# Performance work log

Hardware: AMD Instinct MI355X
Metric: run time of the kernel (lower is better)

## Reference

```python
import jax, jax.numpy as jnp
import numpy as np

B, T, E, D, OUT = 128, 64, 256, 256, 1  # batch, timesteps, encoder_hidden, decoder_hidden, out_feats


def setup_inputs() -> dict:
    key = jax.random.key(0)
    ks = jax.random.split(key, 14)
    s = 0.05
    return {
        "input_encoded": jax.random.normal(ks[0], (B, T, E), jnp.float32),
        "y_history": jax.random.normal(ks[1], (B, T - 1, OUT), jnp.float32),
        # attn_layer: Linear(2D+E -> E), Tanh, Linear(E -> 1)
        "W_a1": jax.random.normal(ks[2], (E, 2 * D + E), jnp.float32) * s,
        "b_a1": jax.random.normal(ks[3], (E,), jnp.float32) * s,
        "W_a2": jax.random.normal(ks[4], (1, E), jnp.float32) * s,
        "b_a2": jax.random.normal(ks[5], (1,), jnp.float32) * s,
        # fc: Linear(E + out_feats -> out_feats)
        "W_fc": jax.random.normal(ks[6], (OUT, E + OUT), jnp.float32) * s,
        "b_fc": jax.random.normal(ks[7], (OUT,), jnp.float32) * s,
        # LSTM(input_size=out_feats, hidden_size=D), gate order i,f,g,o
        "W_ih": jax.random.normal(ks[8], (4 * D, OUT), jnp.float32) * s,
        "W_hh": jax.random.normal(ks[9], (4 * D, D), jnp.float32) * s,
        "b_ih": jax.random.normal(ks[10], (4 * D,), jnp.float32) * s,
        "b_hh": jax.random.normal(ks[11], (4 * D,), jnp.float32) * s,
        # fc_final: Linear(D + E -> 2) (probabilistic=True)
        "W_ff": jax.random.normal(ks[12], (2, D + E), jnp.float32) * s,
        "b_ff": jax.random.normal(ks[13], (2,), jnp.float32) * s,
    }


def reference(input_encoded, y_history, W_a1, b_a1, W_a2, b_a2, W_fc, b_fc,
              W_ih, W_hh, b_ih, b_hh, W_ff, b_ff):
    Bn, Tn, En = input_encoded.shape
    Dn = W_hh.shape[1]

    def step(carry, y_t):
        h, c, _ = carry  # h, c: [B, D]
        # concat(hidden, cell, enc) broadcast over the T encoder positions -> [B, T, 2D+E]
        feats = jnp.concatenate([
            jnp.broadcast_to(h[:, None, :], (Bn, Tn, Dn)),
            jnp.broadcast_to(c[:, None, :], (Bn, Tn, Dn)),
            input_encoded,
        ], axis=2)
        scores = jnp.tanh(feats @ W_a1.T + b_a1) @ W_a2.T + b_a2  # [B, T, 1]
        attn = jax.nn.softmax(scores[..., 0], axis=1)              # [B, T]
        context = jnp.einsum('bt,bte->be', attn, input_encoded)   # [B, E]
        y_tilde = jnp.concatenate([context, y_t], axis=1) @ W_fc.T + b_fc  # [B, 1]
        # single LSTM step, PyTorch gate order (i, f, g, o)
        gates = y_tilde @ W_ih.T + b_ih + h @ W_hh.T + b_hh       # [B, 4D]
        i, f, g, o = jnp.split(gates, 4, axis=1)
        c_new = jax.nn.sigmoid(f) * c + jax.nn.sigmoid(i) * jnp.tanh(g)
        h_new = jax.nn.sigmoid(o) * jnp.tanh(c_new)
        return (h_new, c_new, context), None

    h0 = jnp.zeros((Bn, Dn), input_encoded.dtype)
    c0 = jnp.zeros((Bn, Dn), input_encoded.dtype)
    ctx0 = jnp.zeros((Bn, En), input_encoded.dtype)
    # data_integration=True: loop runs T-1 steps over y_history
    (h, c, context), _ = jax.lax.scan(step, (h0, c0, ctx0), jnp.swapaxes(y_history, 0, 1))
    return jnp.concatenate([h, context], axis=1) @ W_ff.T + b_ff  # [B, 2]
```

## Files before the change

### kernel.cpp

```cpp
#include <hip/hip_runtime.h>
#include <math.h>

#define BATCH 128
#define TENC  64
#define NSTEP 63

#define OFF_WA1ET  0
#define OFF_EPT    65536
#define OFF_PKH    2162688
#define OFF_SX     2359296
#define OFF_HX     2375680
#define OFF_FLAGS  2408448

#define SF 0
#define AF 1
#define CF 2
#define GF 3

typedef __attribute__((ext_vector_type(8))) _Float16 h8_t;
typedef __attribute__((ext_vector_type(2))) _Float16 h2_t;

#if defined(__has_builtin)
#if __has_builtin(__builtin_amdgcn_fdot2)
#define FDOT2(a, b, c) __builtin_amdgcn_fdot2((a), (b), (c), false)
#endif
#endif
#ifndef FDOT2
#define FDOT2(a, b, c) ((c) + (float)(a)[0] * (float)(b)[0] + (float)(a)[1] * (float)(b)[1])
#endif

__device__ __forceinline__ h2_t h2of(h8_t v, int i) {
    h2_t r = {v[2 * i], v[2 * i + 1]};
    return r;
}
__device__ __forceinline__ float ftanh(float x) {
    x = fminf(15.f, fmaxf(-15.f, x));
    float e = __expf(2.f * x);
    return (e - 1.f) * __builtin_amdgcn_rcpf(e + 1.f);
}
__device__ __forceinline__ float fsig(float x) {
    return __builtin_amdgcn_rcpf(1.f + __expf(-x));
}
__device__ __forceinline__ unsigned pack_hc(float h, float c) {
    unsigned short hu = __builtin_bit_cast(unsigned short, (_Float16)h);
    unsigned short cu = __builtin_bit_cast(unsigned short, (_Float16)c);
    return (unsigned)hu | ((unsigned)cu << 16);
}
#define FENCE() asm volatile("" ::: "memory")
#define LGKM0() asm volatile("s_waitcnt lgkmcnt(0)" ::: "memory")

__global__ void pack_weights(const float* __restrict__ Wa1,
                             const float* __restrict__ Whh,
                             float* __restrict__ ws) {
    int idx = blockIdx.x * blockDim.x + threadIdx.x;
    _Float16* PKH = (_Float16*)(ws + OFF_PKH);
    if (idx < 131072) {
        int m = idx & 7, j7 = (idx >> 3) & 127, it = (idx >> 10) & 7;
        int seg = (idx >> 13) & 1, kc = (idx >> 14) & 3, hp = (idx >> 16) & 1;
        int owner = seg ? (1 - hp) : hp;
        int idx256 = kc * 64 + it * 8 + m;
        int k = (idx256 < 128) ? owner * 128 + idx256
                               : 256 + owner * 128 + (idx256 - 128);
        int j = hp * 128 + j7;
        PKH[idx] = (_Float16)Wa1[j * 768 + k];
    } else if (idx < 393216) {
        int n = idx - 131072;
        int m = n & 7, qp = (n >> 3) & 511, kh = (n >> 12) & 1, kk = (n >> 13) & 15, h1 = n >> 17;
        int q = ((qp >> 7) << 8) + h1 * 128 + (qp & 127);
        int k = kh * 128 + kk * 8 + m;
        PKH[131072 + n] = (_Float16)Whh[q * 256 + k];
    } else if (idx < 458752) {
        int n = idx - 393216;
        int k = n >> 8, j = n & 255;
        ws[OFF_WA1ET + n] = Wa1[j * 768 + 512 + k];
    }
}

__global__ void zero_flags(float* __restrict__ ws) {
    unsigned* f = (unsigned*)(ws + OFF_FLAGS);
    f[threadIdx.x] = 0u;
}

__global__ void enc_proj_kernel(const float* __restrict__ enc,
                                const float* __restrict__ ba1,
                                float* __restrict__ ws) {
    __shared__ float smem[8448];
    const int b  = blockIdx.x >> 1;
    const int th = blockIdx.x & 1;
    const int t0 = th * 32;
    const int tid = threadIdx.x;

    const float* encb = enc + (b * TENC + t0) * 256;
    for (int c = 0; c < 32; ++c) smem[c * 256 + tid] = encb[c * 256 + tid];
    __syncthreads();

    const int w = tid >> 6, l = tid & 63;
    float acc[8][4];
    #pragma unroll
    for (int a = 0; a < 8; ++a)
        #pragma unroll
        for (int c = 0; c < 4; ++c) acc[a][c] = 0.f;

    const float4* WT = (const float4*)(ws + OFF_WA1ET);
    for (int k = 0; k < 256; ++k) {
        float4 wv = WT[k * 64 + l];
        #pragma unroll
        for (int tt = 0; tt < 8; ++tt) {
            float e = smem[(w * 8 + tt) * 256 + k];
            acc[tt][0] += e * wv.x; acc[tt][1] += e * wv.y;
            acc[tt][2] += e * wv.z; acc[tt][3] += e * wv.w;
        }
    }
    float4 bb = ((const float4*)ba1)[l];
    __syncthreads();
    #pragma unroll
    for (int tt = 0; tt < 8; ++tt) {
        smem[(4 * l + 0) * 33 + w * 8 + tt] = acc[tt][0] + bb.x;
        smem[(4 * l + 1) * 33 + w * 8 + tt] = acc[tt][1] + bb.y;
        smem[(4 * l + 2) * 33 + w * 8 + tt] = acc[tt][2] + bb.z;
        smem[(4 * l + 3) * 33 + w * 8 + tt] = acc[tt][3] + bb.w;
    }
    __syncthreads();
    float* EPT = ws + OFF_EPT + b * 16384;
    for (int c = 0; c < 32; ++c) {
        int i = c * 256 + tid;
        int j = i >> 5, t5 = i & 31;
        EPT[j * 64 + t0 + t5] = smem[j * 33 + t5];
    }
}

__global__ __launch_bounds__(1024, 4) void decoder_main(
    const float* __restrict__ enc, const float* __restrict__ yhist,
    const float* __restrict__ Wa2,
    const float* __restrict__ Wfc, const float* __restrict__ bfc,
    const float* __restrict__ wih, const float* __restrict__ bih,
    const float* __restrict__ bhh,
    const float* __restrict__ Wff, const float* __restrict__ bff,
    float* __restrict__ ws, float* __restrict__ out) {

    __shared__ float hc[512];
    __shared__ _Float16 hcf16[512] __attribute__((aligned(16)));
    __shared__ float red1[512];
    __shared__ float red2[512];
    __shared__ float g2[512];
    __shared__ float attnw[64];
    __shared__ float encw[64];
    __shared__ float wa2s[128];
    __shared__ float ys[64];
    __shared__ unsigned fl[4];
    __shared__ h8_t  wc[7168] __attribute__((aligned(16)));
    __shared__ float epl[8192];

    const int bid  = blockIdx.x;
    const int b    = bid & 127;
    const int h1   = bid >> 7;
    const int tid  = threadIdx.x;

    const _Float16* PKH = (const _Float16*)(ws + OFF_PKH);
    const float* EPTb = ws + OFF_EPT + b * 16384 + h1 * 8192;
    const float* encb = enc + b * 16384;

    if (tid < 512) { hc[tid] = 0.f; hcf16[tid] = (_Float16)0.f; }
    if (tid < 128) wa2s[tid] = Wa2[h1 * 128 + tid];
    if (tid < NSTEP) ys[tid] = yhist[b * NSTEP + tid];
    if (tid < 4) fl[tid] = 0u;
    {
        float* scr = (float*)wc;
        const int t = tid >> 4, cch = tid & 15;
        float p = 0.f;
        #pragma unroll
        for (int i = 0; i < 16; ++i)
            p += encb[t * 256 + cch * 16 + i] * Wfc[cch * 16 + i];
        scr[t * 16 + cch] = p;
    }
    __syncthreads();
    if (tid < 64) {
        float s = 0.f;
        #pragma unroll
        for (int c = 0; c < 16; ++c) s += ((float*)wc)[tid * 16 + c];
        encw[tid] = s;
    }
    __syncthreads();
    #pragma unroll
    for (int i = 0; i < 8; ++i) epl[i * 1024 + tid] = EPTb[i * 1024 + tid];
    const h8_t* PKGown = (const h8_t*)(PKH + 131072) + h1 * 16384;
    #pragma unroll
    for (int kk = 0; kk < 7; ++kk) wc[kk * 1024 + tid] = PKGown[kk * 1024 + tid];
    const float bfc0  = bfc[0];
    const float wfc_y = Wfc[256];
    float wii = 0.f, wif = 0.f, wig = 0.f, wio = 0.f;
    float bsi = 0.f, bsf = 0.f, bsg = 0.f, bso = 0.f;
    if (tid < 128) {
        const int q0 = h1 * 128 + tid;
        wii = wih[q0];       bsi = bih[q0]       + bhh[q0];
        wif = wih[256 + q0]; bsf = bih[256 + q0] + bhh[256 + q0];
        wig = wih[512 + q0]; bsg = bih[512 + q0] + bhh[512 + q0];
        wio = wih[768 + q0]; bso = bih[768 + q0] + bhh[768 + q0];
    }
    __syncthreads();

    const int j7 = tid & 127, kc = (tid >> 7) & 3;
    const h8_t* W1a = (const h8_t*)PKH + ((h1 * 4 + kc) * 2 + 0) * 1024 + j7;
    const h8_t* W1b = W1a + 1024;
    const _Float16* hb_own  = hcf16 + ((kc < 2) ? h1 * 128 + kc * 64
                                                : 256 + h1 * 128 + (kc - 2) * 64);
    const _Float16* hb_peer = hcf16 + ((kc < 2) ? (1 - h1) * 128 + kc * 64
                                                : 256 + (1 - h1) * 128 + (kc - 2) * 64);
    const h8_t* W4 = PKGown + (tid - 512);

    float*    SXown  = ws + OFF_SX + (b * 2 + h1) * 64;
    float*    SXpeer = ws + OFF_SX + (b * 2 + (1 - h1)) * 64;
    unsigned* HXown  = (unsigned*)(ws + OFF_HX) + (b * 2 + h1) * 128;
    unsigned* HXpeer = (unsigned*)(ws + OFF_HX) + (b * 2 + (1 - h1)) * 128;
    unsigned* FLGown  = (unsigned*)(ws + OFF_FLAGS) + (b * 2 + h1) * 2;
    unsigned* FLGpeer = (unsigned*)(ws + OFF_FLAGS) + (b * 2 + (1 - h1)) * 2;

    for (int step = 0; step < NSTEP; ++step) {
        const unsigned tgt = (unsigned)(step + 1);
        if (tid < 512) {
            float a0 = 0.f, a1 = 0.f;
            #pragma unroll 4
            for (int it = 0; it < 8; ++it) {
                h8_t w  = W1a[it * 128];
                h8_t hv = *(const h8_t*)(hb_own + it * 8);
                a0 = FDOT2(h2of(w, 0), h2of(hv, 0), a0);
                a1 = FDOT2(h2of(w, 1), h2of(hv, 1), a1);
                a0 = FDOT2(h2of(w, 2), h2of(hv, 2), a0);
                a1 = FDOT2(h2of(w, 3), h2of(hv, 3), a1);
            }
            if (step) {
                while (atomicAdd(&fl[SF], 0u) < 2u * (unsigned)step)
                    __builtin_amdgcn_s_sleep(1);
                FENCE();
            }
            #pragma unroll 4
            for (int it = 0; it < 8; ++it) {
                h8_t w  = W1b[it * 128];
                h8_t hv = *(const h8_t*)(hb_peer + it * 8);
                a0 = FDOT2(h2of(w, 0), h2of(hv, 0), a0);
                a1 = FDOT2(h2of(w, 1), h2of(hv, 1), a1);
                a0 = FDOT2(h2of(w, 2), h2of(hv, 2), a0);
                a1 = FDOT2(h2of(w, 3), h2of(hv, 3), a1);
            }
            red1[kc * 128 + j7] = a0 + a1;
            LGKM0();
            if ((tid & 63) == 0) atomicAdd(&fl[AF], 1u);
            while (atomicAdd(&fl[AF], 0u) < 8u * tgt) __builtin_amdgcn_s_sleep(1);
            FENCE();
            {
                const int jc = tid >> 6, lane = tid & 63;
                float partial = 0.f;
                #pragma unroll
                for (int jj = 0; jj < 16; ++jj) {
                    const int j = jc * 16 + jj;
                    float zj = red1[j] + red1[128 + j] + red1[256 + j] + red1[384 + j];
                    float v = epl[j * 64 + lane] + zj;
                    partial += ftanh(v) * wa2s[j];
                }
                red2[jc * 64 + lane] = partial;
            }
            LGKM0();
            if ((tid & 63) == 0) atomicAdd(&fl[CF], 1u);
            if (tid < 128) {
                const int lane = tid & 63;
                while (atomicAdd(&fl[CF], 0u) < 8u * tgt) __builtin_amdgcn_s_sleep(1);
                FENCE();
                float s = 0.f;
                #pragma unroll
                for (int jc2 = 0; jc2 < 8; ++jc2) s += red2[jc2 * 64 + lane];
                if (tid < 64) {
                    atomicExch(&SXown[lane], s);
                    asm volatile("s_waitcnt vmcnt(0)" ::: "memory");
                    if (lane == 0) atomicExch(&FLGown[1], tgt);
                }
                while (atomicAdd(&FLGpeer[1], 0u) < tgt) __builtin_amdgcn_s_sleep(1);
                FENCE();
                s += atomicAdd(&SXpeer[lane], 0.f);
                float m = s;
                #pragma unroll
                for (int d = 32; d >= 1; d >>= 1) m = fmaxf(m, __shfl_xor(m, d));
                float e = __expf(s - m);
                float su = e;
                #pragma unroll
                for (int d = 32; d >= 1; d >>= 1) su += __shfl_xor(su, d);
                float a = e * __builtin_amdgcn_rcpf(su);
                if (tid < 64) attnw[lane] = a;
                float yp = a * encw[lane];
                #pragma unroll
                for (int d = 32; d >= 1; d >>= 1) yp += __shfl_xor(yp, d);
                const float ytil = yp + wfc_y * ys[step] + bfc0;
                while (atomicAdd(&fl[GF], 0u) < 8u * tgt) __builtin_amdgcn_s_sleep(1);
                FENCE();
                float gi = g2[tid]       + ytil * wii + bsi;
                float gf = g2[128 + tid] + ytil * wif + bsf;
                float gg = g2[256 + tid] + ytil * wig + bsg;
                float go = g2[384 + tid] + ytil * wio + bso;
                const int ih = h1 * 128 + tid;
                float co = hc[256 + ih];
                float cn = fsig(gf) * co + fsig(gi) * ftanh(gg);
                float hn = fsig(go) * ftanh(cn);
                hc[ih] = hn; hc[256 + ih] = cn;
                hcf16[ih] = (_Float16)hn; hcf16[256 + ih] = (_Float16)cn;
                atomicExch(&HXown[tid], pack_hc(hn, cn));
            }
        } else {
            const int u2 = tid - 512;
            if (step) {
                if (u2 < 128) {
                    while (atomicAdd(&FLGpeer[0], 0u) < (unsigned)step)
                        __builtin_amdgcn_s_sleep(1);
                    FENCE();
                    unsigned uu = atomicAdd(&HXpeer[u2], 0u);
                    _Float16 hv16 = __builtin_bit_cast(_Float16, (unsigned short)(uu & 0xffffu));
                    _Float16 cv16 = __builtin_bit_cast(_Float16, (unsigned short)(uu >> 16));
                    const int ih = (1 - h1) * 128 + u2;
                    hcf16[ih] = hv16; hcf16[256 + ih] = cv16;
                    hc[ih] = (float)hv16;
                    LGKM0();
                    if ((u2 & 63) == 0) atomicAdd(&fl[SF], 1u);
                }
                while (atomicAdd(&fl[SF], 0u) < 2u * (unsigned)step)
                    __builtin_amdgcn_s_sleep(1);
                FENCE();
            }
            float ga = 0.f, gb = 0.f;
            #pragma unroll
            for (int kk = 0; kk < 7; ++kk) {
                h8_t w0  = wc[kk * 1024 + u2];
                h8_t w1  = wc[kk * 1024 + 512 + u2];
                h8_t hv0 = *(const h8_t*)(hcf16 + kk * 8);
                h8_t hv1 = *(const h8_t*)(hcf16 + 128 + kk * 8);
                ga = FDOT2(h2of(w0, 0), h2of(hv0, 0), ga);
                gb = FDOT2(h2of(w1, 0), h2of(hv1, 0), gb);
                ga = FDOT2(h2of(w0, 1), h2of(hv0, 1), ga);
                gb = FDOT2(h2of(w1, 1), h2of(hv1, 1), gb);
                ga = FDOT2(h2of(w0, 2), h2of(hv0, 2), ga);
                gb = FDOT2(h2of(w1, 2), h2of(hv1, 2), gb);
                ga = FDOT2(h2of(w0, 3), h2of(hv0, 3), ga);
                gb = FDOT2(h2of(w1, 3), h2of(hv1, 3), gb);
            }
            #pragma unroll 3
            for (int kk = 7; kk < 16; ++kk) {
                h8_t w0  = W4[kk * 1024];
                h8_t w1  = W4[kk * 1024 + 512];
                h8_t hv0 = *(const h8_t*)(hcf16 + kk * 8);
                h8_t hv1 = *(const h8_t*)(hcf16 + 128 + kk * 8);
                ga = FDOT2(h2of(w0, 0), h2of(hv0, 0), ga);
                gb = FDOT2(h2of(w1, 0), h2of(hv1, 0), gb);
                ga = FDOT2(h2of(w0, 1), h2of(hv0, 1), ga);
                gb = FDOT2(h2of(w1, 1), h2of(hv1, 1), gb);
                ga = FDOT2(h2of(w0, 2), h2of(hv0, 2), ga);
                gb = FDOT2(h2of(w1, 2), h2of(hv1, 2), gb);
                ga = FDOT2(h2of(w0, 3), h2of(hv0, 3), ga);
                gb = FDOT2(h2of(w1, 3), h2of(hv1, 3), gb);
            }
            g2[u2] = ga + gb;
            LGKM0();
            if ((u2 & 63) == 0) atomicAdd(&fl[GF], 1u);
        }
        __syncthreads();
        if (tid == 0) atomicExch(&FLGown[0], tgt);
    }

    if (tid == 0) {
        while (atomicAdd(&FLGpeer[0], 0u) < (unsigned)NSTEP) { __builtin_amdgcn_s_sleep(1); }
    }
    __syncthreads();
    if (tid < 128) {
        unsigned uu = atomicAdd(&HXpeer[tid], 0u);
        _Float16 hv16 = __builtin_bit_cast(_Float16, (unsigned short)(uu & 0xffffu));
        hc[(1 - h1) * 128 + tid] = (float)hv16;
    }
    __syncthreads();

    if (h1 == 0) {
        if (tid < 256) {
            float cv = 0.f;
            #pragma unroll 8
            for (int t = 0; t < TENC; ++t)
                cv += attnw[t] * encb[t * 256 + tid];
            red1[tid] = cv;
        }
        __syncthreads();
        if (tid < 128) {
            const int wvv = tid >> 6, lane = tid & 63;
            float partial = 0.f;
            #pragma unroll
            for (int qq = 0; qq < 8; ++qq) {
                const int e2 = qq * 64 + lane;
                float v = (e2 < 256) ? hc[e2] : red1[e2 - 256];
                partial += v * Wff[wvv * 512 + e2];
            }
            #pragma unroll
            for (int d = 32; d >= 1; d >>= 1) partial += __shfl_xor(partial, d);
            if (lane == 0) out[b * 2 + wvv] = partial + bff[wvv];
        }
    }
}

extern "C" void kernel_launch(void* const* d_in, const int* in_sizes, int n_in,
                              void* d_out, int out_size, void* d_ws, size_t ws_size,
                              hipStream_t stream) {
    const float* enc = (const float*)d_in[0];
    const float* yh  = (const float*)d_in[1];
    const float* Wa1 = (const float*)d_in[2];
    const float* ba1 = (const float*)d_in[3];
    const float* Wa2 = (const float*)d_in[4];
    const float* Wfc = (const float*)d_in[6];
    const float* bfc = (const float*)d_in[7];
    const float* Wih = (const float*)d_in[8];
    const float* Whh = (const float*)d_in[9];
    const float* bih = (const float*)d_in[10];
    const float* bhh = (const float*)d_in[11];
    const float* Wff = (const float*)d_in[12];
    const float* bff = (const float*)d_in[13];
    float* ws  = (float*)d_ws;
    float* out = (float*)d_out;

    hipLaunchKernelGGL(pack_weights, dim3(1792), dim3(256), 0, stream, Wa1, Whh, ws);
    hipLaunchKernelGGL(zero_flags, dim3(1), dim3(512), 0, stream, ws);
    hipLaunchKernelGGL(enc_proj_kernel, dim3(256), dim3(256), 0, stream, enc, ba1, ws);
    hipLaunchKernelGGL(decoder_main, dim3(256), dim3(1024), 0, stream,
                       enc, yh, Wa2, Wfc, bfc, Wih, bih, bhh, Wff, bff, ws, out);
}
```

Before: 398.8 us.

## Compute full attention scores per block to drop cross-block score exchange

Each block of the pair now computes the attention pre-activation for all 256 hidden units itself. Half the threads handle the block's own h/c slice as soon as it is ready, and the other half handle the peer's slice once it arrives. This removes the per-step global exchange of partial scores (the SX buffer and its flag handshake) and the per-step __syncthreads, replacing them with LDS flag counters and double-buffered h/c exchange. The encoder projection is held as fp16 in LDS to fit, and the LDS weight cache is moved from the LSTM matrix to the peer's attention weights. This trades more redundant compute per block and lower precision for fewer inter-block round trips on the critical path.

Result: slower. 466.1 us (+16.9%).

```diff
diff --git a/kernel.cpp b/kernel.cpp
--- a/kernel.cpp
+++ b/kernel.cpp
@@ -8,14 +8,15 @@
 #define OFF_WA1ET  0
 #define OFF_EPT    65536
 #define OFF_PKH    2162688
-#define OFF_SX     2359296
-#define OFF_HX     2375680
-#define OFF_FLAGS  2408448
+#define OFF_HX     2359296
+#define OFF_FLAGS  2424832
 
 #define SF 0
 #define AF 1
 #define CF 2
 #define GF 3
+#define UF 4
+#define HF 5
 
 typedef __attribute__((ext_vector_type(8))) _Float16 h8_t;
 typedef __attribute__((ext_vector_type(2))) _Float16 h2_t;
@@ -55,13 +56,10 @@
     int idx = blockIdx.x * blockDim.x + threadIdx.x;
     _Float16* PKH = (_Float16*)(ws + OFF_PKH);
     if (idx < 131072) {
-        int m = idx & 7, j7 = (idx >> 3) & 127, it = (idx >> 10) & 7;
-        int seg = (idx >> 13) & 1, kc = (idx >> 14) & 3, hp = (idx >> 16) & 1;
-        int owner = seg ? (1 - hp) : hp;
-        int idx256 = kc * 64 + it * 8 + m;
-        int k = (idx256 < 128) ? owner * 128 + idx256
-                               : 256 + owner * 128 + (idx256 - 128);
-        int j = hp * 128 + j7;
+        int m = idx & 7, j = (idx >> 3) & 255, it = (idx >> 11) & 31, ks = idx >> 16;
+        int idx256 = it * 8 + m;
+        int k = (idx256 < 128) ? ks * 128 + idx256
+                               : 256 + ks * 128 + (idx256 - 128);
         PKH[idx] = (_Float16)Wa1[j * 768 + k];
     } else if (idx < 393216) {
         int n = idx - 131072;
@@ -145,11 +143,11 @@
     __shared__ float g2[512];
     __shared__ float attnw[64];
     __shared__ float encw[64];
-    __shared__ float wa2s[128];
+    __shared__ float wa2s[256];
     __shared__ float ys[64];
-    __shared__ unsigned fl[4];
+    __shared__ unsigned fl[8];
     __shared__ h8_t  wc[7168] __attribute__((aligned(16)));
-    __shared__ float epl[8192];
+    __shared__ _Float16 epl[16384] __attribute__((aligned(16)));
 
     const int bid  = blockIdx.x;
     const int b    = bid & 127;
@@ -157,13 +155,13 @@
     const int tid  = threadIdx.x;
 
     const _Float16* PKH = (const _Float16*)(ws + OFF_PKH);
-    const float* EPTb = ws + OFF_EPT + b * 16384 + h1 * 8192;
+    const float* EPTb = ws + OFF_EPT + b * 16384;
     const float* encb = enc + b * 16384;
 
     if (tid < 512) { hc[tid] = 0.f; hcf16[tid] = (_Float16)0.f; }
-    if (tid < 128) wa2s[tid] = Wa2[h1 * 128 + tid];
+    if (tid < 256) wa2s[tid] = Wa2[tid];
     if (tid < NSTEP) ys[tid] = yhist[b * NSTEP + tid];
-    if (tid < 4) fl[tid] = 0u;
+    if (tid < 8) fl[tid] = 0u;
     {
         float* scr = (float*)wc;
         const int t = tid >> 4, cch = tid & 15;
@@ -182,10 +180,11 @@
     }
     __syncthreads();
     #pragma unroll
-    for (int i = 0; i < 8; ++i) epl[i * 1024 + tid] = EPTb[i * 1024 + tid];
-    const h8_t* PKGown = (const h8_t*)(PKH + 131072) + h1 * 16384;
+    for (int i = 0; i < 16; ++i)
+        epl[i * 1024 + tid] = (_Float16)EPTb[i * 1024 + tid];
+    const h8_t* W1pBase = (const h8_t*)PKH + (1 - h1) * 8192;
     #pragma unroll
-    for (int kk = 0; kk < 7; ++kk) wc[kk * 1024 + tid] = PKGown[kk * 1024 + tid];
+    for (int i = 0; i < 7; ++i) wc[i * 1024 + tid] = W1pBase[i * 1024 + tid];
     const float bfc0  = bfc[0];
     const float wfc_y = Wfc[256];
     float wii = 0.f, wif = 0.f, wig = 0.f, wio = 0.f;
@@ -199,19 +198,13 @@
     }
     __syncthreads();
 
-    const int j7 = tid & 127, kc = (tid >> 7) & 3;
-    const h8_t* W1a = (const h8_t*)PKH + ((h1 * 4 + kc) * 2 + 0) * 1024 + j7;
-    const h8_t* W1b = W1a + 1024;
-    const _Float16* hb_own  = hcf16 + ((kc < 2) ? h1 * 128 + kc * 64
-                                                : 256 + h1 * 128 + (kc - 2) * 64);
-    const _Float16* hb_peer = hcf16 + ((kc < 2) ? (1 - h1) * 128 + kc * 64
-                                                : 256 + (1 - h1) * 128 + (kc - 2) * 64);
+    const int j8 = tid & 255;
+    const h8_t* W1o = (const h8_t*)PKH + h1 * 8192 + j8;
+    const h8_t* W1p = W1pBase + j8;
+    const h8_t* PKGown = (const h8_t*)(PKH + 131072) + h1 * 16384;
     const h8_t* W4 = PKGown + (tid - 512);
 
-    float*    SXown  = ws + OFF_SX + (b * 2 + h1) * 64;
-    float*    SXpeer = ws + OFF_SX + (b * 2 + (1 - h1)) * 64;
-    unsigned* HXown  = (unsigned*)(ws + OFF_HX) + (b * 2 + h1) * 128;
-    unsigned* HXpeer = (unsigned*)(ws + OFF_HX) + (b * 2 + (1 - h1)) * 128;
+    unsigned* HXbase = (unsigned*)(ws + OFF_HX);
     unsigned* FLGown  = (unsigned*)(ws + OFF_FLAGS) + (b * 2 + h1) * 2;
     unsigned* FLGpeer = (unsigned*)(ws + OFF_FLAGS) + (b * 2 + (1 - h1)) * 2;
 
@@ -219,45 +212,81 @@
         const unsigned tgt = (unsigned)(step + 1);
         if (tid < 512) {
             float a0 = 0.f, a1 = 0.f;
-            #pragma unroll 4
-            for (int it = 0; it < 8; ++it) {
-                h8_t w  = W1a[it * 128];
-                h8_t hv = *(const h8_t*)(hb_own + it * 8);
-                a0 = FDOT2(h2of(w, 0), h2of(hv, 0), a0);
-                a1 = FDOT2(h2of(w, 1), h2of(hv, 1), a1);
-                a0 = FDOT2(h2of(w, 2), h2of(hv, 2), a0);
-                a1 = FDOT2(h2of(w, 3), h2of(hv, 3), a1);
-            }
-            if (step) {
+            if (tid < 256) {
+                while (atomicAdd(&fl[UF], 0u) < 2u * (unsigned)step)
+                    __builtin_amdgcn_s_sleep(1);
+                FENCE();
+                const _Float16* hv_h = hcf16 + h1 * 128;
+                const _Float16* hv_c = hcf16 + 256 + h1 * 128;
+                #pragma unroll 4
+                for (int it = 0; it < 16; ++it) {
+                    h8_t w  = W1o[it * 256];
+                    h8_t hv = *(const h8_t*)(hv_h + it * 8);
+                    a0 = FDOT2(h2of(w, 0), h2of(hv, 0), a0);
+                    a1 = FDOT2(h2of(w, 1), h2of(hv, 1), a1);
+                    a0 = FDOT2(h2of(w, 2), h2of(hv, 2), a0);
+                    a1 = FDOT2(h2of(w, 3), h2of(hv, 3), a1);
+                }
+                #pragma unroll 4
+                for (int it = 0; it < 16; ++it) {
+                    h8_t w  = W1o[(16 + it) * 256];
+                    h8_t hv = *(const h8_t*)(hv_c + it * 8);
+                    a0 = FDOT2(h2of(w, 0), h2of(hv, 0), a0);
+                    a1 = FDOT2(h2of(w, 1), h2of(hv, 1), a1);
+                    a0 = FDOT2(h2of(w, 2), h2of(hv, 2), a0);
+                    a1 = FDOT2(h2of(w, 3), h2of(hv, 3), a1);
+                }
+                red1[j8] = a0 + a1;
+            } else {
                 while (atomicAdd(&fl[SF], 0u) < 2u * (unsigned)step)
                     __builtin_amdgcn_s_sleep(1);
                 FENCE();
-            }
-            #pragma unroll 4
-            for (int it = 0; it < 8; ++it) {
-                h8_t w  = W1b[it * 128];
-                h8_t hv = *(const h8_t*)(hb_peer + it * 8);
-                a0 = FDOT2(h2of(w, 0), h2of(hv, 0), a0);
-                a1 = FDOT2(h2of(w, 1), h2of(hv, 1), a1);
-                a0 = FDOT2(h2of(w, 2), h2of(hv, 2), a0);
-                a1 = FDOT2(h2of(w, 3), h2of(hv, 3), a1);
-            }
-            red1[kc * 128 + j7] = a0 + a1;
+                const _Float16* hv_h = hcf16 + (1 - h1) * 128;
+                const _Float16* hv_c = hcf16 + 256 + (1 - h1) * 128;
+                #pragma unroll 4
+                for (int it = 0; it < 16; ++it) {
+                    h8_t w  = wc[it * 256 + j8];
+                    h8_t hv = *(const h8_t*)(hv_h + it * 8);
+                    a0 = FDOT2(h2of(w, 0), h2of(hv, 0), a0);
+                    a1 = FDOT2(h2of(w, 1), h2of(hv, 1), a1);
+                    a0 = FDOT2(h2of(w, 2), h2of(hv, 2), a0);
+                    a1 = FDOT2(h2of(w, 3), h2of(hv, 3), a1);
+                }
+                #pragma unroll 4
+                for (int it = 16; it < 28; ++it) {
+                    h8_t w  = wc[it * 256 + j8];
+                    h8_t hv = *(const h8_t*)(hv_c + (it - 16) * 8);
+                    a0 = FDOT2(h2of(w, 0), h2of(hv, 0), a0);
+                    a1 = FDOT2(h2of(w, 1), h2of(hv, 1), a1);
+                    a0 = FDOT2(h2of(w, 2), h2of(hv, 2), a0);
+                    a1 = FDOT2(h2of(w, 3), h2of(hv, 3), a1);
+                }
+                #pragma unroll
+                for (int it = 28; it < 32; ++it) {
+                    h8_t w  = W1p[it * 256];
+                    h8_t hv = *(const h8_t*)(hv_c + (it - 16) * 8);
+                    a0 = FDOT2(h2of(w, 0), h2of(hv, 0), a0);
+                    a1 = FDOT2(h2of(w, 1), h2of(hv, 1), a1);
+                    a0 = FDOT2(h2of(w, 2), h2of(hv, 2), a0);
+                    a1 = FDOT2(h2of(w, 3), h2of(hv, 3), a1);
+                }
+                red1[256 + j8] = a0 + a1;
+            }
             LGKM0();
             if ((tid & 63) == 0) atomicAdd(&fl[AF], 1u);
             while (atomicAdd(&fl[AF], 0u) < 8u * tgt) __builtin_amdgcn_s_sleep(1);
             FENCE();
             {
-                const int jc = tid >> 6, lane = tid & 63;
+                const int w = tid >> 6, lane = tid & 63;
                 float partial = 0.f;
-                #pragma unroll
-                for (int jj = 0; jj < 16; ++jj) {
-                    const int j = jc * 16 + jj;
-                    float zj = red1[j] + red1[128 + j] + red1[256 + j] + red1[384 + j];
-                    float v = epl[j * 64 + lane] + zj;
+                #pragma unroll 8
+                for (int jj = 0; jj < 32; ++jj) {
+                    const int j = w * 32 + jj;
+                    float zj = red1[j] + red1[256 + j];
+                    float v = (float)epl[j * 64 + lane] + zj;
                     partial += ftanh(v) * wa2s[j];
                 }
-                red2[jc * 64 + lane] = partial;
+                red2[w * 64 + lane] = partial;
             }
             LGKM0();
             if ((tid & 63) == 0) atomicAdd(&fl[CF], 1u);
@@ -267,15 +296,7 @@
                 FENCE();
                 float s = 0.f;
                 #pragma unroll
-                for (int jc2 = 0; jc2 < 8; ++jc2) s += red2[jc2 * 64 + lane];
-                if (tid < 64) {
-                    atomicExch(&SXown[lane], s);
-                    asm volatile("s_waitcnt vmcnt(0)" ::: "memory");
-                    if (lane == 0) atomicExch(&FLGown[1], tgt);
-                }
-                while (atomicAdd(&FLGpeer[1], 0u) < tgt) __builtin_amdgcn_s_sleep(1);
-                FENCE();
-                s += atomicAdd(&SXpeer[lane], 0.f);
+                for (int w2 = 0; w2 < 8; ++w2) s += red2[w2 * 64 + lane];
                 float m = s;
                 #pragma unroll
                 for (int d = 32; d >= 1; d >>= 1) m = fmaxf(m, __shfl_xor(m, d));
@@ -301,16 +322,29 @@
                 float hn = fsig(go) * ftanh(cn);
                 hc[ih] = hn; hc[256 + ih] = cn;
                 hcf16[ih] = (_Float16)hn; hcf16[256 + ih] = (_Float16)cn;
-                atomicExch(&HXown[tid], pack_hc(hn, cn));
+                LGKM0();
+                if ((tid & 63) == 0) atomicAdd(&fl[UF], 1u);
+                unsigned* HXownP = HXbase + (((step & 1) * 128 + b) * 2 + h1) * 128;
+                atomicExch(&HXownP[tid], pack_hc(hn, cn));
+                asm volatile("s_waitcnt vmcnt(0)" ::: "memory");
+                if ((tid & 63) == 0) atomicAdd(&fl[HF], 1u);
+                if (tid == 0) {
+                    while (atomicAdd(&fl[HF], 0u) < 2u * tgt) __builtin_amdgcn_s_sleep(1);
+                    atomicExch(&FLGown[0], tgt);
+                }
             }
         } else {
             const int u2 = tid - 512;
-            if (step) {
-                if (u2 < 128) {
+            if (u2 < 128) {
+                if (step) {
                     while (atomicAdd(&FLGpeer[0], 0u) < (unsigned)step)
                         __builtin_amdgcn_s_sleep(1);
                     FENCE();
-                    unsigned uu = atomicAdd(&HXpeer[u2], 0u);
+                    while (atomicAdd(&fl[UF], 0u) < 2u * (unsigned)step)
+                        __builtin_amdgcn_s_sleep(1);
+                    FENCE();
+                    unsigned* HXpeerP = HXbase + ((((step - 1) & 1) * 128 + b) * 2 + (1 - h1)) * 128;
+                    unsigned uu = atomicAdd(&HXpeerP[u2], 0u);
                     _Float16 hv16 = __builtin_bit_cast(_Float16, (unsigned short)(uu & 0xffffu));
                     _Float16 cv16 = __builtin_bit_cast(_Float16, (unsigned short)(uu >> 16));
                     const int ih = (1 - h1) * 128 + u2;
@@ -319,28 +353,15 @@
                     LGKM0();
                     if ((u2 & 63) == 0) atomicAdd(&fl[SF], 1u);
                 }
+            }
+            if (step) {
                 while (atomicAdd(&fl[SF], 0u) < 2u * (unsigned)step)
                     __builtin_amdgcn_s_sleep(1);
                 FENCE();
             }
             float ga = 0.f, gb = 0.f;
-            #pragma unroll
-            for (int kk = 0; kk < 7; ++kk) {
-                h8_t w0  = wc[kk * 1024 + u2];
-                h8_t w1  = wc[kk * 1024 + 512 + u2];
-                h8_t hv0 = *(const h8_t*)(hcf16 + kk * 8);
-                h8_t hv1 = *(const h8_t*)(hcf16 + 128 + kk * 8);
-                ga = FDOT2(h2of(w0, 0), h2of(hv0, 0), ga);
-                gb = FDOT2(h2of(w1, 0), h2of(hv1, 0), gb);
-                ga = FDOT2(h2of(w0, 1), h2of(hv0, 1), ga);
-                gb = FDOT2(h2of(w1, 1), h2of(hv1, 1), gb);
-                ga = FDOT2(h2of(w0, 2), h2of(hv0, 2), ga);
-                gb = FDOT2(h2of(w1, 2), h2of(hv1, 2), gb);
-                ga = FDOT2(h2of(w0, 3), h2of(hv0, 3), ga);
-                gb = FDOT2(h2of(w1, 3), h2of(hv1, 3), gb);
-            }
             #pragma unroll 3
-            for (int kk = 7; kk < 16; ++kk) {
+            for (int kk = 0; kk < 16; ++kk) {
                 h8_t w0  = W4[kk * 1024];
                 h8_t w1  = W4[kk * 1024 + 512];
                 h8_t hv0 = *(const h8_t*)(hcf16 + kk * 8);
@@ -358,16 +379,16 @@
             LGKM0();
             if ((u2 & 63) == 0) atomicAdd(&fl[GF], 1u);
         }
-        __syncthreads();
-        if (tid == 0) atomicExch(&FLGown[0], tgt);
-    }
-
+    }
+
+    __syncthreads();
     if (tid == 0) {
         while (atomicAdd(&FLGpeer[0], 0u) < (unsigned)NSTEP) { __builtin_amdgcn_s_sleep(1); }
     }
     __syncthreads();
     if (tid < 128) {
-        unsigned uu = atomicAdd(&HXpeer[tid], 0u);
+        unsigned* HXpeerF = HXbase + ((((NSTEP - 1) & 1) * 128 + b) * 2 + (1 - h1)) * 128;
+        unsigned uu = atomicAdd(&HXpeerF[tid], 0u);
         _Float16 hv16 = __builtin_bit_cast(_Float16, (unsigned short)(uu & 0xffffu));
         hc[(1 - h1) * 128 + tid] = (float)hv16;
     }
```
